# Kernel tuning notes

Measured on AMD Instinct MI355X. Metric: run time of the kernel, lower is better.

The kernel has to match this reference:

```python
import jax, jax.numpy as jnp
import numpy as np

DIM = 128
NUM_HEADS = 8
HEAD_DIM = DIM // NUM_HEADS
SCALE = HEAD_DIM ** -0.5


def setup_inputs() -> dict:
    key = jax.random.key(0)
    k0, k1, k2, k3 = jax.random.split(key, 4)
    B, N, C, H, W = 4, 8, DIM, 96, 96
    features = jax.random.normal(k0, (B, N, C, H, W), dtype=jnp.float32)
    w_qkv = jax.random.normal(k1, (C, 3 * C), dtype=jnp.float32) * (C ** -0.5)
    w_proj = jax.random.normal(k2, (C, C), dtype=jnp.float32) * (C ** -0.5)
    b_proj = jax.random.normal(k3, (C,), dtype=jnp.float32) * 0.02
    gamma = jnp.ones((C,), dtype=jnp.float32)
    beta = jnp.zeros((C,), dtype=jnp.float32)
    return {"features": features, "w_qkv": w_qkv, "w_proj": w_proj,
            "b_proj": b_proj, "gamma": gamma, "beta": beta}


def _layernorm(x, gamma, beta, eps=1e-5):
    mu = jnp.mean(x, axis=-1, keepdims=True)
    var = jnp.mean(jnp.square(x - mu), axis=-1, keepdims=True)
    return (x - mu) * jax.lax.rsqrt(var + eps) * gamma + beta


def reference(features, w_qkv, w_proj, b_proj, gamma, beta):
    B, N, C, H, W = features.shape
    residual = features
    # (B,N,C,H,W) -> (B*H*W, N, C)
    x = jnp.transpose(features, (0, 3, 4, 1, 2)).reshape(B * H * W, N, C)
    x = _layernorm(x, gamma, beta)
    qkv = (x @ w_qkv).reshape(B * H * W, N, 3, NUM_HEADS, HEAD_DIM)
    qkv = jnp.transpose(qkv, (2, 0, 3, 1, 4))  # (3, P, h, N, d)
    q, k, v = qkv[0], qkv[1], qkv[2]
    attn = jnp.einsum('phnd,phmd->phnm', q, k) * SCALE
    attn = jax.nn.softmax(attn, axis=-1)
    out = jnp.einsum('phnm,phmd->phnd', attn, v)  # (P, h, N, d)
    out = jnp.transpose(out, (0, 2, 1, 3)).reshape(B * H * W, N, C)
    out = out @ w_proj + b_proj
    out = out.reshape(B, H, W, N, C).transpose(0, 3, 4, 1, 2)
    return residual + out
```

## Files before the change

### kernel.cpp

```cpp
#include <hip/hip_runtime.h>

#define NFR 8
#define CDIM 128
#define HH 96
#define WW 96
#define NB 4
#define HWSZ 9216
#define NBLK 2304
#define NXCD 8
#define CPX (NBLK / NXCD)

typedef __attribute__((ext_vector_type(8))) short bf16x8;
typedef __attribute__((ext_vector_type(4))) float f32x4;
typedef __attribute__((ext_vector_type(2))) float f32x2;
typedef __attribute__((ext_vector_type(2))) __bf16 bf16x2;

union FragU { uint4 u; bf16x8 v; };

__device__ inline float bf2f(unsigned short h) {
    unsigned int x = ((unsigned int)h) << 16;
    float f; __builtin_memcpy(&f, &x, 4); return f;
}
__device__ inline unsigned short f2bf(float f) {
    unsigned int x; __builtin_memcpy(&x, &f, 4);
    return (unsigned short)((x + 0x7FFFu + ((x >> 16) & 1u)) >> 16);
}
__device__ inline unsigned int packbf(float a, float b) {
    return (unsigned int)f2bf(a) | ((unsigned int)f2bf(b) << 16);
}
__device__ inline unsigned int cvt2(float a, float b) {
    f32x2 f = {a, b};
    bf16x2 h = __builtin_convertvector(f, bf16x2);
    unsigned int u; __builtin_memcpy(&u, &h, 4); return u;
}
__device__ inline unsigned short cvt1(float a) {
    __bf16 h = (__bf16)a;
    unsigned short s; __builtin_memcpy(&s, &h, 2); return s;
}
__device__ inline int posmap(int c5) {
    return (c5 < 16) ? (((c5 >> 2) << 3) + (c5 & 3))
                     : ((((c5 & 15) >> 2) << 3) + 4 + (c5 & 3));
}

__global__ __launch_bounds__(256)
void repack_k(const float* __restrict__ wqkv, const float* __restrict__ wproj,
              const float* __restrict__ gamma, const float* __restrict__ beta,
              unsigned short* __restrict__ ws)
{
    int gid = blockIdx.x * 256 + threadIdx.x;
    uint4* wsq = (uint4*)ws;
    int l = gid & 63, lr = l & 15, lg = (l >> 4) & 3;
    if (gid < 8192) {
        int unit = gid >> 6;
        int col, ks, stride;
        float scale = 1.0f;
        const float* src;
        if (unit < 64) {
            int t = unit >> 2; ks = unit & 3;
            int hd = t >> 1, three = t & 1;
            col = three * 128 + hd * 16 + lr;
            src = wqkv; stride = 384;
            if (three == 0) scale = 0.25f;
        } else if (unit < 96) {
            int u2 = unit - 64; int hd = u2 >> 2; ks = u2 & 3;
            col = 256 + hd * 16 + lr;
            src = wqkv; stride = 384;
        } else {
            int u3 = unit - 96; int nt = u3 >> 2; ks = u3 & 3;
            col = nt * 16 + lr;
            src = wproj; stride = 128;
        }
        unsigned int dw[4];
        #pragma unroll
        for (int i = 0; i < 4; ++i) {
            int e0 = 2 * i, e1 = 2 * i + 1;
            int c0 = ks * 32 + lg * 4 + (e0 & 3) + ((e0 >> 2) << 4);
            int c1 = ks * 32 + lg * 4 + (e1 & 3) + ((e1 >> 2) << 4);
            dw[i] = packbf(src[c0 * stride + col] * scale, src[c1 * stride + col] * scale);
        }
        uint4 o; o.x = dw[0]; o.y = dw[1]; o.z = dw[2]; o.w = dw[3];
        wsq[gid] = o;
    } else if (gid < 8192 + 32) {
        int t = gid - 8192;
        int isb = t >> 4;
        int unit = t & 15;
        int ks2 = unit >> 2, lg2 = unit & 3;
        const float* src2 = isb ? beta : gamma;
        unsigned int dw[4];
        #pragma unroll
        for (int i = 0; i < 4; ++i) {
            int e0 = 2 * i, e1 = 2 * i + 1;
            int c0 = ks2 * 32 + lg2 * 4 + (e0 & 3) + ((e0 >> 2) << 4);
            int c1 = ks2 * 32 + lg2 * 4 + (e1 & 3) + ((e1 >> 2) << 4);
            dw[i] = packbf(src2[c0], src2[c1]);
        }
        uint4 o; o.x = dw[0]; o.y = dw[1]; o.z = dw[2]; o.w = dw[3];
        wsq[8192 + t] = o;
    }
}

__device__ inline f32x4 attn_ov(f32x4 q, f32x4 k, f32x4 v, bool valid) {
    FragU qb, kb, vb;
    qb.u.x = cvt2(q.x, q.y); qb.u.y = cvt2(q.z, q.w); qb.u.z = 0; qb.u.w = 0;
    kb.u.x = cvt2(k.x, k.y); kb.u.y = cvt2(k.z, k.w); kb.u.z = 0; kb.u.w = 0;
    vb.u.x = cvt2(v.x, v.y); vb.u.y = cvt2(v.z, v.w); vb.u.z = 0; vb.u.w = 0;
    f32x4 zz = {0,0,0,0};
    f32x4 st = __builtin_amdgcn_mfma_f32_16x16x32_bf16(kb.v, qb.v, zz, 0, 0, 0);
    float sc0 = st.x, sc1 = st.y, sc2 = st.z, sc3 = st.w;
    float m = valid ? fmaxf(fmaxf(sc0, sc1), fmaxf(sc2, sc3)) : -3.0e38f;
    m = fmaxf(m, __shfl_xor(m, 16));
    float e0 = valid ? __expf(sc0 - m) : 0.f, e1 = valid ? __expf(sc1 - m) : 0.f;
    float e2 = valid ? __expf(sc2 - m) : 0.f, e3 = valid ? __expf(sc3 - m) : 0.f;
    float sm = e0 + e1 + e2 + e3; sm += __shfl_xor(sm, 16);
    float inv = 1.f / sm;
    FragU pb;
    pb.u.x = cvt2(valid ? e0 * inv : 0.f, valid ? e1 * inv : 0.f);
    pb.u.y = cvt2(valid ? e2 * inv : 0.f, valid ? e3 * inv : 0.f);
    pb.u.z = 0; pb.u.w = 0;
    return __builtin_amdgcn_mfma_f32_16x16x32_bf16(vb.v, pb.v, zz, 0, 0, 0);
}

__device__ inline void ln_reg(FragU* xf, const uint4* gf, const uint4* bfr) {
    float s = 0.f, ss = 0.f;
    #pragma unroll
    for (int ks = 0; ks < 4; ++ks) {
        const unsigned short* e = (const unsigned short*)&xf[ks];
        #pragma unroll
        for (int j = 0; j < 8; ++j) { float x = bf2f(e[j]); s += x; ss += x * x; }
    }
    s += __shfl_xor(s, 16); ss += __shfl_xor(ss, 16);
    s += __shfl_xor(s, 32); ss += __shfl_xor(ss, 32);
    float mu = s * (1.f / 128.f);
    float var = ss * (1.f / 128.f) - mu * mu;
    float rstd = rsqrtf(var + 1e-5f);
    float mr = mu * rstd;
    #pragma unroll
    for (int ks = 0; ks < 4; ++ks) {
        const unsigned short* e = (const unsigned short*)&xf[ks];
        const unsigned short* g = (const unsigned short*)&gf[ks];
        const unsigned short* b = (const unsigned short*)&bfr[ks];
        unsigned int dw[4];
        #pragma unroll
        for (int i = 0; i < 4; ++i) {
            float x0 = bf2f(e[2 * i])     * rstd - mr;
            float x1 = bf2f(e[2 * i + 1]) * rstd - mr;
            dw[i] = cvt2(x0 * bf2f(g[2 * i])     + bf2f(b[2 * i]),
                         x1 * bf2f(g[2 * i + 1]) + bf2f(b[2 * i + 1]));
        }
        xf[ks].u.x = dw[0]; xf[ks].u.y = dw[1]; xf[ks].u.z = dw[2]; xf[ks].u.w = dw[3];
    }
}

__global__ __launch_bounds__(256, 3)
void cfa_main(const float* __restrict__ feat, const float* __restrict__ bproj,
              const unsigned short* __restrict__ ws, float* __restrict__ outp)
{
    __shared__ uint4 xlnU4[2048];
    unsigned short* xln16 = (unsigned short*)xlnU4;
    unsigned int*   xln32 = (unsigned int*)xlnU4;

    const int tid = threadIdx.x;
    const int blk = (int)(blockIdx.x % NXCD) * CPX + (int)blockIdx.x / NXCD;
    const int wt = blk % 6, h = (blk / 6) % 96, b = blk / (6 * 96);
    const int base = ((b * NFR) * CDIM) * HWSZ + h * WW + wt * 16;

    #pragma unroll
    for (int it = 0; it < 8; ++it) {
        int t = it * 256 + tid;
        int pq = t & 3;
        int pr = t >> 2;
        int n = pr >> 6;
        int c = (pr & 63) * 2;
        const float* src = feat + base + (n * CDIM + c) * HWSZ + pq * 4;
        float4 f0 = *(const float4*)src;
        float4 f1 = *(const float4*)(src + HWSZ);
        int ks = c >> 5;
        int pos = posmap(c & 31);
        const float* a0 = (const float*)&f0;
        const float* a1 = (const float*)&f1;
        #pragma unroll
        for (int j = 0; j < 4; ++j) {
            int p = pq * 4 + j;
            int g = p >> 3, pin = p & 7;
            xln32[(g * 8192 + ks * 2048 + (pin * 8 + n) * 32 + pos) >> 1] =
                cvt2(a0[j], a1[j]);
        }
    }
    __syncthreads();

    const int wv = tid >> 6, l = tid & 63, lr = l & 15, lg = l >> 4;
    const uint4* wsq = (const uint4*)ws;

    uint4 Ac[4], Bc[4], Vc[4], gf[4], bfx[4];
    #pragma unroll
    for (int ks = 0; ks < 4; ++ks) {
        Ac[ks] = wsq[(0 * 8 + ks) * 64 + l];
        Bc[ks] = wsq[(0 * 8 + 4 + ks) * 64 + l];
        Vc[ks] = wsq[4096 + ks * 64 + l];
        gf[ks]  = wsq[8192 + ks * 4 + lg];
        bfx[ks] = wsq[8208 + ks * 4 + lg];
    }

    FragU xf0[4], xf1[4];
    #pragma unroll
    for (int ks = 0; ks < 4; ++ks) {
        xf0[ks].u = xlnU4[ks * 256 + (wv * 16 + lr) * 4 + lg];
        xf1[ks].u = xlnU4[1024 + ks * 256 + (wv * 16 + lr) * 4 + lg];
    }
    ln_reg(xf0, gf, bfx);
    ln_reg(xf1, gf, bfx);

    const bool valid = ((lg >> 1) == (lr >> 3));
    FragU pa0[4], pa1[4];
    #pragma unroll
    for (int ks = 0; ks < 4; ++ks) {
        pa0[ks].u.x = 0; pa0[ks].u.y = 0; pa0[ks].u.z = 0; pa0[ks].u.w = 0;
        pa1[ks].u.x = 0; pa1[ks].u.y = 0; pa1[ks].u.z = 0; pa1[ks].u.w = 0;
    }

    uint4 PBc[4];
    float biasc;
    #pragma unroll
    for (int hd = 0; hd < 8; ++hd) {
        uint4 An[4], Bn[4], Vn[4];
        if (hd < 7) {
            #pragma unroll
            for (int ks = 0; ks < 4; ++ks) {
                An[ks] = wsq[((hd + 1) * 8 + ks) * 64 + l];
                Bn[ks] = wsq[((hd + 1) * 8 + 4 + ks) * 64 + l];
                Vn[ks] = wsq[4096 + ((hd + 1) * 4 + ks) * 64 + l];
            }
        } else {
            #pragma unroll
            for (int ks = 0; ks < 4; ++ks) PBc[ks] = wsq[6144 + ks * 64 + l];
            biasc = bproj[lr];
        }
        f32x4 q0 = {0,0,0,0}, k0 = {0,0,0,0}, v0 = {0,0,0,0};
        f32x4 q1 = {0,0,0,0}, k1 = {0,0,0,0}, v1 = {0,0,0,0};
        #pragma unroll
        for (int ks = 0; ks < 4; ++ks) {
            FragU A, B, V2; A.u = Ac[ks]; B.u = Bc[ks]; V2.u = Vc[ks];
            q0 = __builtin_amdgcn_mfma_f32_16x16x32_bf16(A.v,  xf0[ks].v, q0, 0, 0, 0);
            k0 = __builtin_amdgcn_mfma_f32_16x16x32_bf16(B.v,  xf0[ks].v, k0, 0, 0, 0);
            q1 = __builtin_amdgcn_mfma_f32_16x16x32_bf16(A.v,  xf1[ks].v, q1, 0, 0, 0);
            k1 = __builtin_amdgcn_mfma_f32_16x16x32_bf16(B.v,  xf1[ks].v, k1, 0, 0, 0);
            v0 = __builtin_amdgcn_mfma_f32_16x16x32_bf16(xf0[ks].v, V2.v, v0, 0, 0, 0);
            v1 = __builtin_amdgcn_mfma_f32_16x16x32_bf16(xf1[ks].v, V2.v, v1, 0, 0, 0);
        }
        f32x4 o0 = attn_ov(q0, k0, v0, valid);
        f32x4 o1 = attn_ov(q1, k1, v1, valid);
        if ((hd & 1) == 0) {
            pa0[hd >> 1].u.x = cvt2(o0.x, o0.y); pa0[hd >> 1].u.y = cvt2(o0.z, o0.w);
            pa1[hd >> 1].u.x = cvt2(o1.x, o1.y); pa1[hd >> 1].u.y = cvt2(o1.z, o1.w);
        } else {
            pa0[hd >> 1].u.z = cvt2(o0.x, o0.y); pa0[hd >> 1].u.w = cvt2(o0.z, o0.w);
            pa1[hd >> 1].u.z = cvt2(o1.x, o1.y); pa1[hd >> 1].u.w = cvt2(o1.z, o1.w);
        }
        if (hd < 7) {
            #pragma unroll
            for (int ks = 0; ks < 4; ++ks) { Ac[ks] = An[ks]; Bc[ks] = Bn[ks]; Vc[ks] = Vn[ks]; }
        }
    }

    __syncthreads();

    unsigned short* out_t = xln16;
    #pragma unroll
    for (int nt = 0; nt < 8; ++nt) {
        uint4 PBn[4]; float biasn;
        if (nt < 7) {
            #pragma unroll
            for (int ks = 0; ks < 4; ++ks) PBn[ks] = wsq[6144 + ((nt + 1) * 4 + ks) * 64 + l];
            biasn = bproj[(nt + 1) * 16 + lr];
        }
        f32x4 a0 = {0,0,0,0}, a1 = {0,0,0,0};
        #pragma unroll
        for (int ks = 0; ks < 4; ++ks) {
            FragU B; B.u = PBc[ks];
            a0 = __builtin_amdgcn_mfma_f32_16x16x32_bf16(pa0[ks].v, B.v, a0, 0, 0, 0);
            a1 = __builtin_amdgcn_mfma_f32_16x16x32_bf16(pa1[ks].v, B.v, a1, 0, 0, 0);
        }
        int col = nt * 16 + lr;
        #pragma unroll
        for (int j = 0; j < 4; ++j) {
            int row = wv * 16 + lg * 4 + j;
            int n = row & 7, p = row >> 3;
            out_t[n * 1024 + (col ^ n) * 8 + p]        = cvt1(a0[j] + biasc);
            out_t[8192 + n * 1024 + (col ^ n) * 8 + p] = cvt1(a1[j] + biasc);
        }
        if (nt < 7) {
            #pragma unroll
            for (int ks = 0; ks < 4; ++ks) PBc[ks] = PBn[ks];
            biasc = biasn;
        }
    }
    __syncthreads();

    #pragma unroll 4
    for (int it = 0; it < 16; ++it) {
        int t = it * 256 + tid;
        int pq = t & 3;
        int row = t >> 2;
        int n = row >> 7, c = row & 127;
        int gaddr = base + (n * CDIM + c) * HWSZ + pq * 4;
        float4 r0 = *(const float4*)(feat + gaddr);
        int p = pq * 4;
        int idx = (p >> 3) * 8192 + n * 1024 + (c ^ n) * 8 + (p & 7);
        uint2 tv = *(const uint2*)(out_t + idx);
        const unsigned short* tp = (const unsigned short*)&tv;
        float4 o;
        o.x = r0.x + bf2f(tp[0]); o.y = r0.y + bf2f(tp[1]);
        o.z = r0.z + bf2f(tp[2]); o.w = r0.w + bf2f(tp[3]);
        *(float4*)(outp + gaddr) = o;
    }
}

extern "C" void kernel_launch(void* const* d_in, const int* in_sizes, int n_in,
                              void* d_out, int out_size, void* d_ws, size_t ws_size,
                              hipStream_t stream) {
    const float* feat  = (const float*)d_in[0];
    const float* wqkv  = (const float*)d_in[1];
    const float* wproj = (const float*)d_in[2];
    const float* bproj = (const float*)d_in[3];
    const float* gamma = (const float*)d_in[4];
    const float* beta  = (const float*)d_in[5];
    unsigned short* ws = (unsigned short*)d_ws;
    float* outp = (float*)d_out;

    hipLaunchKernelGGL(repack_k, dim3(33), dim3(256), 0, stream,
                       wqkv, wproj, gamma, beta, ws);
    hipLaunchKernelGGL(cfa_main, dim3(NBLK), dim3(256), 0, stream,
                       feat, bproj, ws, outp);
}
```

Baseline: 111.2 us.

## Stage per-head QKV weight fragments through double-buffered LDS shared across waves

Previously each of the four waves loaded the full set of 12 weight fragments per head from global memory into registers. Now each wave loads 3 of the 12 fragments, writes them into a double-buffered region of shared memory, and all waves read the fragments back from LDS after a block barrier each head iteration. This cuts redundant global/L2 weight traffic by 4x and lowers register pressure, at the cost of extra LDS reads and writes plus a __syncthreads per head. It reuses the xln LDS region after the LayerNorm fragments have been read into registers.

```diff
diff --git a/kernel.cpp b/kernel.cpp
--- a/kernel.cpp
+++ b/kernel.cpp
@@ -151,6 +151,10 @@
     }
 }
 
+__device__ inline int wslot(int hd, int s) {
+    return (s < 8) ? (hd * 8 + s) * 64 : 4096 + (hd * 4 + (s - 8)) * 64;
+}
+
 __global__ __launch_bounds__(256, 3)
 void cfa_main(const float* __restrict__ feat, const float* __restrict__ bproj,
               const unsigned short* __restrict__ ws, float* __restrict__ outp)
@@ -191,12 +195,9 @@
     const int wv = tid >> 6, l = tid & 63, lr = l & 15, lg = l >> 4;
     const uint4* wsq = (const uint4*)ws;
 
-    uint4 Ac[4], Bc[4], Vc[4], gf[4], bfx[4];
-    #pragma unroll
-    for (int ks = 0; ks < 4; ++ks) {
-        Ac[ks] = wsq[(0 * 8 + ks) * 64 + l];
-        Bc[ks] = wsq[(0 * 8 + 4 + ks) * 64 + l];
-        Vc[ks] = wsq[4096 + ks * 64 + l];
+    uint4 gf[4], bfx[4];
+    #pragma unroll
+    for (int ks = 0; ks < 4; ++ks) {
         gf[ks]  = wsq[8192 + ks * 4 + lg];
         bfx[ks] = wsq[8208 + ks * 4 + lg];
     }
@@ -210,6 +211,17 @@
     ln_reg(xf0, gf, bfx);
     ln_reg(xf1, gf, bfx);
 
+    __syncthreads();
+
+    {
+        uint4 s0 = wsq[wslot(0, wv * 3 + 0) + l];
+        uint4 s1 = wsq[wslot(0, wv * 3 + 1) + l];
+        uint4 s2 = wsq[wslot(0, wv * 3 + 2) + l];
+        xlnU4[512 + (wv * 3 + 0) * 64 + l] = s0;
+        xlnU4[512 + (wv * 3 + 1) * 64 + l] = s1;
+        xlnU4[512 + (wv * 3 + 2) * 64 + l] = s2;
+    }
+
     const bool valid = ((lg >> 1) == (lr >> 3));
     FragU pa0[4], pa1[4];
     #pragma unroll
@@ -222,14 +234,13 @@
     float biasc;
     #pragma unroll
     for (int hd = 0; hd < 8; ++hd) {
-        uint4 An[4], Bn[4], Vn[4];
+        __syncthreads();
+        const uint4* buf = &xlnU4[(hd & 1) ? 1280 : 512];
+        uint4 sn0, sn1, sn2;
         if (hd < 7) {
-            #pragma unroll
-            for (int ks = 0; ks < 4; ++ks) {
-                An[ks] = wsq[((hd + 1) * 8 + ks) * 64 + l];
-                Bn[ks] = wsq[((hd + 1) * 8 + 4 + ks) * 64 + l];
-                Vn[ks] = wsq[4096 + ((hd + 1) * 4 + ks) * 64 + l];
-            }
+            sn0 = wsq[wslot(hd + 1, wv * 3 + 0) + l];
+            sn1 = wsq[wslot(hd + 1, wv * 3 + 1) + l];
+            sn2 = wsq[wslot(hd + 1, wv * 3 + 2) + l];
         } else {
             #pragma unroll
             for (int ks = 0; ks < 4; ++ks) PBc[ks] = wsq[6144 + ks * 64 + l];
@@ -239,7 +250,10 @@
         f32x4 q1 = {0,0,0,0}, k1 = {0,0,0,0}, v1 = {0,0,0,0};
         #pragma unroll
         for (int ks = 0; ks < 4; ++ks) {
-            FragU A, B, V2; A.u = Ac[ks]; B.u = Bc[ks]; V2.u = Vc[ks];
+            FragU A, B, V2;
+            A.u  = buf[ks * 64 + l];
+            B.u  = buf[(4 + ks) * 64 + l];
+            V2.u = buf[(8 + ks) * 64 + l];
             q0 = __builtin_amdgcn_mfma_f32_16x16x32_bf16(A.v,  xf0[ks].v, q0, 0, 0, 0);
             k0 = __builtin_amdgcn_mfma_f32_16x16x32_bf16(B.v,  xf0[ks].v, k0, 0, 0, 0);
             q1 = __builtin_amdgcn_mfma_f32_16x16x32_bf16(A.v,  xf1[ks].v, q1, 0, 0, 0);
@@ -257,8 +271,10 @@
             pa1[hd >> 1].u.z = cvt2(o1.x, o1.y); pa1[hd >> 1].u.w = cvt2(o1.z, o1.w);
         }
         if (hd < 7) {
-            #pragma unroll
-            for (int ks = 0; ks < 4; ++ks) { Ac[ks] = An[ks]; Bc[ks] = Bn[ks]; Vc[ks] = Vn[ks]; }
+            int dst = ((hd + 1) & 1) ? 1280 : 512;
+            xlnU4[dst + (wv * 3 + 0) * 64 + l] = sn0;
+            xlnU4[dst + (wv * 3 + 1) * 64 + l] = sn1;
+            xlnU4[dst + (wv * 3 + 2) * 64 + l] = sn2;
         }
     }
 
```

After: 104.7 us. -5.9%, faster.

## Share QKV weight fragments across waves via double-buffered LDS per head pair

Applied to the files above, without the earlier changes.

Previously every wave loaded all QKV weight fragments for each head from global memory (through L2/L1). Now each of the four waves loads a quarter of a head pair's fragments and stores them into a double-buffered LDS region, and all waves read the fragments from LDS for their MFMAs. This cuts redundant global weight traffic by a factor of four. In exchange it adds a barrier per head pair, LDS reads inside the MFMA loop, and grows shared memory from 32KB to 48KB, which may limit the three-blocks-per-CU occupancy target.

```diff
diff --git a/kernel.cpp b/kernel.cpp
--- a/kernel.cpp
+++ b/kernel.cpp
@@ -151,11 +151,18 @@
     }
 }
 
+__device__ inline int wslot(int hd, int s) {
+    return (s < 8) ? (hd * 8 + s) * 64 : 4096 + (hd * 4 + (s - 8)) * 64;
+}
+__device__ inline int wpslot(int hp, int ps) {
+    return wslot(2 * hp + (ps >= 12 ? 1 : 0), ps % 12);
+}
+
 __global__ __launch_bounds__(256, 3)
 void cfa_main(const float* __restrict__ feat, const float* __restrict__ bproj,
               const unsigned short* __restrict__ ws, float* __restrict__ outp)
 {
-    __shared__ uint4 xlnU4[2048];
+    __shared__ uint4 xlnU4[3072];
     unsigned short* xln16 = (unsigned short*)xlnU4;
     unsigned int*   xln32 = (unsigned int*)xlnU4;
 
@@ -191,12 +198,13 @@
     const int wv = tid >> 6, l = tid & 63, lr = l & 15, lg = l >> 4;
     const uint4* wsq = (const uint4*)ws;
 
-    uint4 Ac[4], Bc[4], Vc[4], gf[4], bfx[4];
-    #pragma unroll
-    for (int ks = 0; ks < 4; ++ks) {
-        Ac[ks] = wsq[(0 * 8 + ks) * 64 + l];
-        Bc[ks] = wsq[(0 * 8 + 4 + ks) * 64 + l];
-        Vc[ks] = wsq[4096 + ks * 64 + l];
+    uint4 h0s[6];
+    #pragma unroll
+    for (int i = 0; i < 6; ++i) h0s[i] = wsq[wpslot(0, wv * 6 + i) + l];
+
+    uint4 gf[4], bfx[4];
+    #pragma unroll
+    for (int ks = 0; ks < 4; ++ks) {
         gf[ks]  = wsq[8192 + ks * 4 + lg];
         bfx[ks] = wsq[8208 + ks * 4 + lg];
     }
@@ -210,6 +218,11 @@
     ln_reg(xf0, gf, bfx);
     ln_reg(xf1, gf, bfx);
 
+    __syncthreads();
+
+    #pragma unroll
+    for (int i = 0; i < 6; ++i) xlnU4[(wv * 6 + i) * 64 + l] = h0s[i];
+
     const bool valid = ((lg >> 1) == (lr >> 3));
     FragU pa0[4], pa1[4];
     #pragma unroll
@@ -221,44 +234,50 @@
     uint4 PBc[4];
     float biasc;
     #pragma unroll
-    for (int hd = 0; hd < 8; ++hd) {
-        uint4 An[4], Bn[4], Vn[4];
-        if (hd < 7) {
-            #pragma unroll
-            for (int ks = 0; ks < 4; ++ks) {
-                An[ks] = wsq[((hd + 1) * 8 + ks) * 64 + l];
-                Bn[ks] = wsq[((hd + 1) * 8 + 4 + ks) * 64 + l];
-                Vn[ks] = wsq[4096 + ((hd + 1) * 4 + ks) * 64 + l];
-            }
+    for (int hp = 0; hp < 4; ++hp) {
+        __syncthreads();
+        const uint4* buf = &xlnU4[(hp & 1) ? 1536 : 0];
+        uint4 sn[6];
+        if (hp < 3) {
+            #pragma unroll
+            for (int i = 0; i < 6; ++i) sn[i] = wsq[wpslot(hp + 1, wv * 6 + i) + l];
         } else {
             #pragma unroll
             for (int ks = 0; ks < 4; ++ks) PBc[ks] = wsq[6144 + ks * 64 + l];
             biasc = bproj[lr];
         }
-        f32x4 q0 = {0,0,0,0}, k0 = {0,0,0,0}, v0 = {0,0,0,0};
-        f32x4 q1 = {0,0,0,0}, k1 = {0,0,0,0}, v1 = {0,0,0,0};
-        #pragma unroll
-        for (int ks = 0; ks < 4; ++ks) {
-            FragU A, B, V2; A.u = Ac[ks]; B.u = Bc[ks]; V2.u = Vc[ks];
-            q0 = __builtin_amdgcn_mfma_f32_16x16x32_bf16(A.v,  xf0[ks].v, q0, 0, 0, 0);
-            k0 = __builtin_amdgcn_mfma_f32_16x16x32_bf16(B.v,  xf0[ks].v, k0, 0, 0, 0);
-            q1 = __builtin_amdgcn_mfma_f32_16x16x32_bf16(A.v,  xf1[ks].v, q1, 0, 0, 0);
-            k1 = __builtin_amdgcn_mfma_f32_16x16x32_bf16(B.v,  xf1[ks].v, k1, 0, 0, 0);
-            v0 = __builtin_amdgcn_mfma_f32_16x16x32_bf16(xf0[ks].v, V2.v, v0, 0, 0, 0);
-            v1 = __builtin_amdgcn_mfma_f32_16x16x32_bf16(xf1[ks].v, V2.v, v1, 0, 0, 0);
-        }
-        f32x4 o0 = attn_ov(q0, k0, v0, valid);
-        f32x4 o1 = attn_ov(q1, k1, v1, valid);
-        if ((hd & 1) == 0) {
-            pa0[hd >> 1].u.x = cvt2(o0.x, o0.y); pa0[hd >> 1].u.y = cvt2(o0.z, o0.w);
-            pa1[hd >> 1].u.x = cvt2(o1.x, o1.y); pa1[hd >> 1].u.y = cvt2(o1.z, o1.w);
-        } else {
-            pa0[hd >> 1].u.z = cvt2(o0.x, o0.y); pa0[hd >> 1].u.w = cvt2(o0.z, o0.w);
-            pa1[hd >> 1].u.z = cvt2(o1.x, o1.y); pa1[hd >> 1].u.w = cvt2(o1.z, o1.w);
-        }
-        if (hd < 7) {
-            #pragma unroll
-            for (int ks = 0; ks < 4; ++ks) { Ac[ks] = An[ks]; Bc[ks] = Bn[ks]; Vc[ks] = Vn[ks]; }
+        #pragma unroll
+        for (int hl = 0; hl < 2; ++hl) {
+            const uint4* hb = buf + hl * 12 * 64;
+            f32x4 q0 = {0,0,0,0}, k0 = {0,0,0,0}, v0 = {0,0,0,0};
+            f32x4 q1 = {0,0,0,0}, k1 = {0,0,0,0}, v1 = {0,0,0,0};
+            #pragma unroll
+            for (int ks = 0; ks < 4; ++ks) {
+                FragU A, B, V2;
+                A.u  = hb[ks * 64 + l];
+                B.u  = hb[(4 + ks) * 64 + l];
+                V2.u = hb[(8 + ks) * 64 + l];
+                q0 = __builtin_amdgcn_mfma_f32_16x16x32_bf16(A.v,  xf0[ks].v, q0, 0, 0, 0);
+                k0 = __builtin_amdgcn_mfma_f32_16x16x32_bf16(B.v,  xf0[ks].v, k0, 0, 0, 0);
+                q1 = __builtin_amdgcn_mfma_f32_16x16x32_bf16(A.v,  xf1[ks].v, q1, 0, 0, 0);
+                k1 = __builtin_amdgcn_mfma_f32_16x16x32_bf16(B.v,  xf1[ks].v, k1, 0, 0, 0);
+                v0 = __builtin_amdgcn_mfma_f32_16x16x32_bf16(xf0[ks].v, V2.v, v0, 0, 0, 0);
+                v1 = __builtin_amdgcn_mfma_f32_16x16x32_bf16(xf1[ks].v, V2.v, v1, 0, 0, 0);
+            }
+            f32x4 o0 = attn_ov(q0, k0, v0, valid);
+            f32x4 o1 = attn_ov(q1, k1, v1, valid);
+            if (hl == 0) {
+                pa0[hp].u.x = cvt2(o0.x, o0.y); pa0[hp].u.y = cvt2(o0.z, o0.w);
+                pa1[hp].u.x = cvt2(o1.x, o1.y); pa1[hp].u.y = cvt2(o1.z, o1.w);
+            } else {
+                pa0[hp].u.z = cvt2(o0.x, o0.y); pa0[hp].u.w = cvt2(o0.z, o0.w);
+                pa1[hp].u.z = cvt2(o1.x, o1.y); pa1[hp].u.w = cvt2(o1.z, o1.w);
+            }
+        }
+        if (hp < 3) {
+            uint4* dst = &xlnU4[((hp + 1) & 1) ? 1536 : 0];
+            #pragma unroll
+            for (int i = 0; i < 6; ++i) dst[(wv * 6 + i) * 64 + l] = sn[i];
         }
     }
 
```

New measurement: 162.4 us. +46.1%, slower.
